# Kernel tuning notes

Hardware: AMD Instinct MI355X
Metric: run time of the kernel (lower is better)

The kernel has to match this reference:

```python
import jax, jax.numpy as jnp
import numpy as np


def setup_inputs() -> dict:
    key = jax.random.key(0)
    k1, k2 = jax.random.split(key)
    B, N, D = 256, 50000, 2048
    queries = jax.random.normal(k1, (B, D), dtype=jnp.float32)
    bank = jax.random.normal(k2, (N, D), dtype=jnp.float32)
    return {"queries": queries, "bank": bank}


def reference(queries, bank):
    # Cosine similarity of every query against every bank row, fused as one
    # GEMM + row-norm scaling (original repeats the query N times per item
    # in a Python loop; math is identical).
    eps = jnp.float32(1e-12)
    q_norm = jnp.sqrt(jnp.sum(queries * queries, axis=1, keepdims=True))  # [B,1]
    b_norm = jnp.sqrt(jnp.sum(bank * bank, axis=1))                       # [N]
    dots = jnp.einsum('bd,nd->bn', queries, bank)                         # [B,N]
    scores = dots / jnp.maximum(q_norm * b_norm[None, :], eps)
    best_idx = jnp.argmax(scores, axis=1)  # retrieval result per batch item
    return best_idx, scores
```

## Files before the change

### kernel.cpp

```cpp
#include <hip/hip_runtime.h>
#include <stdint.h>

#define MQ 256
#define NB 50000
#define KD 2048
#define BN 64
#define BK 64
#define KT (KD / BK)
#define NBLK ((NB + BN - 1) / BN)

typedef __attribute__((ext_vector_type(8))) short bf16x8;
typedef __attribute__((ext_vector_type(4))) float f32x4;

__device__ __forceinline__ unsigned int pack_bf16(float a, float b) {
  unsigned int ua = __float_as_uint(a);
  ua += 0x7fffu + ((ua >> 16) & 1u);
  unsigned int ub = __float_as_uint(b);
  ub += 0x7fffu + ((ub >> 16) & 1u);
  return (ua >> 16) | (ub & 0xffff0000u);
}

__device__ __forceinline__ unsigned int ordf(float f) {
  unsigned int u = __float_as_uint(f);
  return (u & 0x80000000u) ? ~u : (u | 0x80000000u);
}
__device__ __forceinline__ float deordf(unsigned int e) {
  unsigned int u = (e & 0x80000000u) ? (e ^ 0x80000000u) : ~e;
  return __uint_as_float(u);
}

__device__ __forceinline__ float wave_sum(float v) {
#pragma unroll
  for (int o = 32; o > 0; o >>= 1) v += __shfl_down(v, o, 64);
  return v;
}

__global__ __launch_bounds__(256) void prep_q(const float* __restrict__ q,
                                              unsigned short* __restrict__ qbf,
                                              float* __restrict__ qn) {
  const int b = blockIdx.x, tid = threadIdx.x;
  const float* row = q + (size_t)b * KD;
  float4 v0 = *(const float4*)(row + tid * 8);
  float4 v1 = *(const float4*)(row + tid * 8 + 4);
  float sq = v0.x * v0.x + v0.y * v0.y + v0.z * v0.z + v0.w * v0.w +
             v1.x * v1.x + v1.y * v1.y + v1.z * v1.z + v1.w * v1.w;
  uint4 o;
  o.x = pack_bf16(v0.x, v0.y);
  o.y = pack_bf16(v0.z, v0.w);
  o.z = pack_bf16(v1.x, v1.y);
  o.w = pack_bf16(v1.z, v1.w);
  *(uint4*)(qbf + (size_t)b * KD + tid * 8) = o;
  sq = wave_sum(sq);
  __shared__ float s4[4];
  if ((tid & 63) == 0) s4[tid >> 6] = sq;
  __syncthreads();
  if (tid == 0) qn[b] = sqrtf(s4[0] + s4[1] + s4[2] + s4[3]);
}

__global__ __launch_bounds__(256, 3) void gemm_scores(
    const float* __restrict__ bank, const unsigned short* __restrict__ qbf,
    const float* __restrict__ qn, float* __restrict__ out_scores,
    unsigned long long* __restrict__ bm) {
  __shared__ alignas(16) unsigned short As[MQ * BK];
  __shared__ alignas(16) unsigned short Bs[BN * BK];
  __shared__ float qn_s[MQ];
  __shared__ float bsq_s[256];
  __shared__ float bn_s[BN];

  const int tid = threadIdx.x;
  const int w = tid >> 6;
  const int lane = tid & 63;
  const int n0 = blockIdx.x * BN;

  qn_s[tid] = qn[tid];

  f32x4 acc[4][4] = {};

  const int br = tid >> 2;
  const int bseg = (tid & 3) * 16;
  int brow = n0 + br;
  if (brow >= NB) brow = NB - 1;
  const float* bsrc = bank + (size_t)brow * KD + bseg;

  const int a_row_in_grp = lane >> 3;
  const int a_colb = (lane & 7) * 8;
  float bsq = 0.f;

  float4 f0 = *(const float4*)(bsrc);
  float4 f1 = *(const float4*)(bsrc + 4);
  float4 f2 = *(const float4*)(bsrc + 8);
  float4 f3 = *(const float4*)(bsrc + 12);

  for (int kt = 0; kt < KT; ++kt) {
    const int k0 = kt * BK;
#pragma unroll
    for (int i = 0; i < 8; ++i) {
      const int row = w * 64 + i * 8 + a_row_in_grp;
      const unsigned short* src = qbf + (size_t)row * KD + k0 + a_colb;
      unsigned short* dst = &As[row * BK + a_colb];
      __builtin_amdgcn_global_load_lds(
          (const __attribute__((address_space(1))) unsigned int*)src,
          (__attribute__((address_space(3))) unsigned int*)dst, 16, 0, 0);
    }
    bsq += f0.x * f0.x + f0.y * f0.y + f0.z * f0.z + f0.w * f0.w +
           f1.x * f1.x + f1.y * f1.y + f1.z * f1.z + f1.w * f1.w +
           f2.x * f2.x + f2.y * f2.y + f2.z * f2.z + f2.w * f2.w +
           f3.x * f3.x + f3.y * f3.y + f3.z * f3.z + f3.w * f3.w;
    uint4 p0, p1;
    p0.x = pack_bf16(f0.x, f0.y);
    p0.y = pack_bf16(f0.z, f0.w);
    p0.z = pack_bf16(f1.x, f1.y);
    p0.w = pack_bf16(f1.z, f1.w);
    p1.x = pack_bf16(f2.x, f2.y);
    p1.y = pack_bf16(f2.z, f2.w);
    p1.z = pack_bf16(f3.x, f3.y);
    p1.w = pack_bf16(f3.z, f3.w);
    *(uint4*)&Bs[br * BK + bseg] = p0;
    *(uint4*)&Bs[br * BK + bseg + 8] = p1;
    __syncthreads();
    if (kt + 1 < KT) {
      const float* p = bsrc + (kt + 1) * BK;
      f0 = *(const float4*)(p);
      f1 = *(const float4*)(p + 4);
      f2 = *(const float4*)(p + 8);
      f3 = *(const float4*)(p + 12);
    }
#pragma unroll
    for (int s = 0; s < 2; ++s) {
      bf16x8 af[4], bfv[4];
#pragma unroll
      for (int t = 0; t < 4; ++t) {
        af[t] = *(const bf16x8*)&As[(w * 64 + t * 16 + (lane & 15)) * BK +
                                    s * 32 + (lane >> 4) * 8];
        bfv[t] = *(const bf16x8*)&Bs[(t * 16 + (lane & 15)) * BK + s * 32 +
                                     (lane >> 4) * 8];
      }
#pragma unroll
      for (int tm = 0; tm < 4; ++tm)
#pragma unroll
        for (int tn = 0; tn < 4; ++tn)
          acc[tm][tn] = __builtin_amdgcn_mfma_f32_16x16x32_bf16(
              af[tm], bfv[tn], acc[tm][tn], 0, 0, 0);
    }
    __syncthreads();
  }

  bsq_s[tid] = bsq;
  __syncthreads();
  if (tid < BN)
    bn_s[tid] = sqrtf(bsq_s[tid * 4] + bsq_s[tid * 4 + 1] + bsq_s[tid * 4 + 2] +
                      bsq_s[tid * 4 + 3]);
  __syncthreads();

  const int quad = lane >> 4, nl = lane & 15;
#pragma unroll
  for (int tm = 0; tm < 4; ++tm) {
#pragma unroll
    for (int r = 0; r < 4; ++r) {
      const int m = w * 64 + tm * 16 + quad * 4 + r;
      const float qm = qn_s[m];
      unsigned long long best = 0ull;
#pragma unroll
      for (int tn = 0; tn < 4; ++tn) {
        const int gn = n0 + tn * 16 + nl;
        if (gn < NB) {
          const float sc =
              acc[tm][tn][r] / fmaxf(qm * bn_s[tn * 16 + nl], 1e-12f);
          out_scores[(size_t)m * NB + gn] = sc;
          const unsigned long long pk =
              ((unsigned long long)ordf(sc) << 32) | (unsigned int)gn;
          best = pk > best ? pk : best;
        }
      }
#pragma unroll
      for (int mask = 1; mask < 16; mask <<= 1) {
        const unsigned long long o = __shfl_xor(best, mask, 64);
        best = o > best ? o : best;
      }
      if (nl == 0) bm[(size_t)m * NBLK + blockIdx.x] = best;
    }
  }
}

__global__ __launch_bounds__(256) void argmax_rescue(
    const unsigned long long* __restrict__ bm, const float* __restrict__ scores,
    const float* __restrict__ q, const float* __restrict__ bank,
    float* __restrict__ out_idx) {
  const int b = blockIdx.x, tid = threadIdx.x;
  const int w = tid >> 6, lane = tid & 63;
  const unsigned long long* rbm = bm + (size_t)b * NBLK;

  unsigned long long pmax = 0ull;
  for (int i = tid; i < NBLK; i += 256) {
    const unsigned long long v = rbm[i];
    pmax = v > pmax ? v : pmax;
  }
#pragma unroll
  for (int o = 32; o > 0; o >>= 1) {
    const unsigned long long v = __shfl_down(pmax, o, 64);
    pmax = v > pmax ? v : pmax;
  }
  __shared__ unsigned long long red[4];
  if (lane == 0) red[w] = pmax;
  __syncthreads();
  unsigned long long gmax = red[0];
#pragma unroll
  for (int i = 1; i < 4; ++i) gmax = red[i] > gmax ? red[i] : gmax;
  const float thr = deordf((unsigned int)(gmax >> 32)) - 2e-3f;

  __shared__ int cand[64];
  __shared__ int cnt;
  if (tid == 0) cnt = 0;
  __syncthreads();
  const float* srow = scores + (size_t)b * NB;
  for (int i = tid; i < NBLK; i += 256) {
    const float bmf = deordf((unsigned int)(rbm[i] >> 32));
    if (bmf >= thr) {
      const int base = i * BN;
      const int lim = min(BN, NB - base);
      for (int j = 0; j < lim; ++j) {
        if (srow[base + j] >= thr) {
          const int c = atomicAdd(&cnt, 1);
          if (c < 64) cand[c] = base + j;
        }
      }
    }
  }
  __syncthreads();
  const int nc = min(cnt, 64);

  __shared__ float dd[4], ss[4];
  float best = -1e30f;
  int bidx = 0x7fffffff;
  const float* qrow = q + (size_t)b * KD;
  for (int c = 0; c < nc; ++c) {
    const int idx = cand[c];
    const float* brow = bank + (size_t)idx * KD;
    float d = 0.f, s = 0.f;
#pragma unroll
    for (int j = 0; j < 8; ++j) {
      const float bv = brow[tid * 8 + j];
      const float qv = qrow[tid * 8 + j];
      d = fmaf(qv, bv, d);
      s = fmaf(bv, bv, s);
    }
    d = wave_sum(d);
    s = wave_sum(s);
    if (lane == 0) {
      dd[w] = d;
      ss[w] = s;
    }
    __syncthreads();
    const float dt = dd[0] + dd[1] + dd[2] + dd[3];
    const float st = ss[0] + ss[1] + ss[2] + ss[3];
    const float sc = dt / fmaxf(sqrtf(st), 1e-12f);
    if (sc > best || (sc == best && idx < bidx)) {
      best = sc;
      bidx = idx;
    }
    __syncthreads();
  }
  if (tid == 0) out_idx[b] = (float)bidx;
}

extern "C" void kernel_launch(void* const* d_in, const int* in_sizes, int n_in,
                              void* d_out, int out_size, void* d_ws,
                              size_t ws_size, hipStream_t stream) {
  const float* queries = (const float*)d_in[0];
  const float* bank = (const float*)d_in[1];
  float* out = (float*)d_out;
  float* out_scores = out + MQ;

  char* ws = (char*)d_ws;
  unsigned short* qbf = (unsigned short*)ws;
  float* qn = (float*)(ws + (size_t)MQ * KD * 2);
  unsigned long long* bm =
      (unsigned long long*)(ws + (size_t)MQ * KD * 2 + 2048);

  prep_q<<<MQ, 256, 0, stream>>>(queries, qbf, qn);
  gemm_scores<<<NBLK, 256, 0, stream>>>(bank, qbf, qn, out_scores, bm);
  argmax_rescue<<<MQ, 256, 0, stream>>>(bm, out_scores, queries, bank, out);
}
```

Measured before the change: 631.3 us.

## XOR-swizzle A/B LDS tiles and hand-tune waitcnt barriers for prefetch overlap

Applies an XOR swizzle to the LDS layout of the query (A) and bank (B) tiles so the MFMA fragment reads avoid bank conflicts. For A, the global source column is permuted while the LDS destination stays linear. The change also replaces __syncthreads with explicit s_waitcnt plus s_barrier and scheduling fences. This lets the next-iteration bank prefetch loads stay in flight (vmcnt(4)) across the barrier instead of being drained. The handwritten waitcnt counts depend on the compiler's load ordering, which risks a correctness fault if that ordering changes.

Result: no change. 627.9 us (-0.5%).

```diff
diff --git a/kernel.cpp b/kernel.cpp
--- a/kernel.cpp
+++ b/kernel.cpp
@@ -11,6 +11,12 @@
 
 typedef __attribute__((ext_vector_type(8))) short bf16x8;
 typedef __attribute__((ext_vector_type(4))) float f32x4;
+
+#define SFENCE()                       \
+  do {                                 \
+    asm volatile("" ::: "memory");     \
+    __builtin_amdgcn_sched_barrier(0); \
+  } while (0)
 
 __device__ __forceinline__ unsigned int pack_bf16(float a, float b) {
   unsigned int ua = __float_as_uint(a);
@@ -78,12 +84,14 @@
 
   const int br = tid >> 2;
   const int bseg = (tid & 3) * 16;
+  const int bkey = (br & 7) * 8;
+  const int be0 = bseg ^ bkey;
   int brow = n0 + br;
   if (brow >= NB) brow = NB - 1;
   const float* bsrc = bank + (size_t)brow * KD + bseg;
 
-  const int a_row_in_grp = lane >> 3;
-  const int a_colb = (lane & 7) * 8;
+  const int arow = lane >> 3;
+  const int acs = ((lane & 7) ^ arow) * 8;
   float bsq = 0.f;
 
   float4 f0 = *(const float4*)(bsrc);
@@ -93,15 +101,17 @@
 
   for (int kt = 0; kt < KT; ++kt) {
     const int k0 = kt * BK;
+    SFENCE();
 #pragma unroll
     for (int i = 0; i < 8; ++i) {
-      const int row = w * 64 + i * 8 + a_row_in_grp;
-      const unsigned short* src = qbf + (size_t)row * KD + k0 + a_colb;
-      unsigned short* dst = &As[row * BK + a_colb];
+      const int row = w * 64 + i * 8 + arow;
+      const unsigned short* src = qbf + (size_t)row * KD + k0 + acs;
+      unsigned short* dst = &As[row * BK + (lane & 7) * 8];
       __builtin_amdgcn_global_load_lds(
           (const __attribute__((address_space(1))) unsigned int*)src,
           (__attribute__((address_space(3))) unsigned int*)dst, 16, 0, 0);
     }
+    SFENCE();
     bsq += f0.x * f0.x + f0.y * f0.y + f0.z * f0.z + f0.w * f0.w +
            f1.x * f1.x + f1.y * f1.y + f1.z * f1.z + f1.w * f1.w +
            f2.x * f2.x + f2.y * f2.y + f2.z * f2.z + f2.w * f2.w +
@@ -115,25 +125,28 @@
     p1.y = pack_bf16(f2.z, f2.w);
     p1.z = pack_bf16(f3.x, f3.y);
     p1.w = pack_bf16(f3.z, f3.w);
-    *(uint4*)&Bs[br * BK + bseg] = p0;
-    *(uint4*)&Bs[br * BK + bseg + 8] = p1;
-    __syncthreads();
+    *(uint4*)&Bs[br * BK + be0] = p0;
+    *(uint4*)&Bs[br * BK + (be0 ^ 8)] = p1;
     if (kt + 1 < KT) {
       const float* p = bsrc + (kt + 1) * BK;
       f0 = *(const float4*)(p);
       f1 = *(const float4*)(p + 4);
       f2 = *(const float4*)(p + 8);
       f3 = *(const float4*)(p + 12);
-    }
+      asm volatile("s_waitcnt vmcnt(4) lgkmcnt(0)" ::: "memory");
+    } else {
+      asm volatile("s_waitcnt vmcnt(0) lgkmcnt(0)" ::: "memory");
+    }
+    __builtin_amdgcn_s_barrier();
+    SFENCE();
 #pragma unroll
     for (int s = 0; s < 2; ++s) {
+      const int kx = (s * 32 + (lane >> 4) * 8) ^ ((lane & 7) * 8);
       bf16x8 af[4], bfv[4];
 #pragma unroll
       for (int t = 0; t < 4; ++t) {
-        af[t] = *(const bf16x8*)&As[(w * 64 + t * 16 + (lane & 15)) * BK +
-                                    s * 32 + (lane >> 4) * 8];
-        bfv[t] = *(const bf16x8*)&Bs[(t * 16 + (lane & 15)) * BK + s * 32 +
-                                     (lane >> 4) * 8];
+        af[t] = *(const bf16x8*)&As[(w * 64 + t * 16 + (lane & 15)) * BK + kx];
+        bfv[t] = *(const bf16x8*)&Bs[(t * 16 + (lane & 15)) * BK + kx];
       }
 #pragma unroll
       for (int tm = 0; tm < 4; ++tm)
@@ -142,7 +155,9 @@
           acc[tm][tn] = __builtin_amdgcn_mfma_f32_16x16x32_bf16(
               af[tm], bfv[tn], acc[tm][tn], 0, 0, 0);
     }
-    __syncthreads();
+    asm volatile("s_waitcnt lgkmcnt(0)" ::: "memory");
+    __builtin_amdgcn_s_barrier();
+    SFENCE();
   }
 
   bsq_s[tid] = bsq;
```

## Double-buffer bank tiles, swizzle LDS, load query fragments directly from global

Applied to the files above, without the earlier changes.

The GEMM main loop now uses a ping-pong LDS buffer for the bf16 bank tile, with one barrier per k-step instead of two. The bank tile layout is XOR-swizzled to reduce LDS bank conflicts. The query operand is no longer staged in LDS; each wave loads its bf16x8 MFMA fragments straight from global memory, which cuts LDS traffic and size but relies on cache hits for data reused across blocks. The rescoring kernel also switches to vectorized float4 loads.

Measured after the change: 689.6 us. 1.09x slower.

```diff
diff --git a/kernel.cpp b/kernel.cpp
--- a/kernel.cpp
+++ b/kernel.cpp
@@ -61,8 +61,7 @@
     const float* __restrict__ bank, const unsigned short* __restrict__ qbf,
     const float* __restrict__ qn, float* __restrict__ out_scores,
     unsigned long long* __restrict__ bm) {
-  __shared__ alignas(16) unsigned short As[MQ * BK];
-  __shared__ alignas(16) unsigned short Bs[BN * BK];
+  __shared__ alignas(16) unsigned short Bs[2][BN * BK];
   __shared__ float qn_s[MQ];
   __shared__ float bsq_s[256];
   __shared__ float bn_s[BN];
@@ -78,30 +77,25 @@
 
   const int br = tid >> 2;
   const int bseg = (tid & 3) * 16;
+  const int be0 = bseg ^ ((br & 7) * 8);
   int brow = n0 + br;
   if (brow >= NB) brow = NB - 1;
   const float* bsrc = bank + (size_t)brow * KD + bseg;
 
-  const int a_row_in_grp = lane >> 3;
-  const int a_colb = (lane & 7) * 8;
+  const int quad4 = lane >> 4;
+  const unsigned short* abase[4];
+#pragma unroll
+  for (int t = 0; t < 4; ++t)
+    abase[t] = qbf + (size_t)(w * 64 + t * 16 + (lane & 15)) * KD + quad4 * 8;
+
   float bsq = 0.f;
-
-  float4 f0 = *(const float4*)(bsrc);
-  float4 f1 = *(const float4*)(bsrc + 4);
-  float4 f2 = *(const float4*)(bsrc + 8);
-  float4 f3 = *(const float4*)(bsrc + 12);
-
-  for (int kt = 0; kt < KT; ++kt) {
-    const int k0 = kt * BK;
-#pragma unroll
-    for (int i = 0; i < 8; ++i) {
-      const int row = w * 64 + i * 8 + a_row_in_grp;
-      const unsigned short* src = qbf + (size_t)row * KD + k0 + a_colb;
-      unsigned short* dst = &As[row * BK + a_colb];
-      __builtin_amdgcn_global_load_lds(
-          (const __attribute__((address_space(1))) unsigned int*)src,
-          (__attribute__((address_space(3))) unsigned int*)dst, 16, 0, 0);
-    }
+  float4 f0, f1, f2, f3;
+
+  f0 = *(const float4*)(bsrc);
+  f1 = *(const float4*)(bsrc + 4);
+  f2 = *(const float4*)(bsrc + 8);
+  f3 = *(const float4*)(bsrc + 12);
+  {
     bsq += f0.x * f0.x + f0.y * f0.y + f0.z * f0.z + f0.w * f0.w +
            f1.x * f1.x + f1.y * f1.y + f1.z * f1.z + f1.w * f1.w +
            f2.x * f2.x + f2.y * f2.y + f2.z * f2.z + f2.w * f2.w +
@@ -115,25 +109,28 @@
     p1.y = pack_bf16(f2.z, f2.w);
     p1.z = pack_bf16(f3.x, f3.y);
     p1.w = pack_bf16(f3.z, f3.w);
-    *(uint4*)&Bs[br * BK + bseg] = p0;
-    *(uint4*)&Bs[br * BK + bseg + 8] = p1;
-    __syncthreads();
-    if (kt + 1 < KT) {
-      const float* p = bsrc + (kt + 1) * BK;
-      f0 = *(const float4*)(p);
-      f1 = *(const float4*)(p + 4);
-      f2 = *(const float4*)(p + 8);
-      f3 = *(const float4*)(p + 12);
-    }
+    *(uint4*)&Bs[0][br * BK + be0] = p0;
+    *(uint4*)&Bs[0][br * BK + (be0 ^ 8)] = p1;
+  }
+  __syncthreads();
+  {
+    const float* p = bsrc + BK;
+    f0 = *(const float4*)(p);
+    f1 = *(const float4*)(p + 4);
+    f2 = *(const float4*)(p + 8);
+    f3 = *(const float4*)(p + 12);
+  }
+
+  for (int kt = 0; kt < KT; ++kt) {
+    const int p = kt & 1;
 #pragma unroll
     for (int s = 0; s < 2; ++s) {
+      const int kx = (s * 32 + quad4 * 8) ^ ((lane & 7) * 8);
       bf16x8 af[4], bfv[4];
 #pragma unroll
       for (int t = 0; t < 4; ++t) {
-        af[t] = *(const bf16x8*)&As[(w * 64 + t * 16 + (lane & 15)) * BK +
-                                    s * 32 + (lane >> 4) * 8];
-        bfv[t] = *(const bf16x8*)&Bs[(t * 16 + (lane & 15)) * BK + s * 32 +
-                                     (lane >> 4) * 8];
+        af[t] = *(const bf16x8*)(abase[t] + kt * BK + s * 32);
+        bfv[t] = *(const bf16x8*)&Bs[p][(t * 16 + (lane & 15)) * BK + kx];
       }
 #pragma unroll
       for (int tm = 0; tm < 4; ++tm)
@@ -142,9 +139,34 @@
           acc[tm][tn] = __builtin_amdgcn_mfma_f32_16x16x32_bf16(
               af[tm], bfv[tn], acc[tm][tn], 0, 0, 0);
     }
-    __syncthreads();
-  }
-
+    if (kt + 1 < KT) {
+      bsq += f0.x * f0.x + f0.y * f0.y + f0.z * f0.z + f0.w * f0.w +
+             f1.x * f1.x + f1.y * f1.y + f1.z * f1.z + f1.w * f1.w +
+             f2.x * f2.x + f2.y * f2.y + f2.z * f2.z + f2.w * f2.w +
+             f3.x * f3.x + f3.y * f3.y + f3.z * f3.z + f3.w * f3.w;
+      uint4 p0, p1;
+      p0.x = pack_bf16(f0.x, f0.y);
+      p0.y = pack_bf16(f0.z, f0.w);
+      p0.z = pack_bf16(f1.x, f1.y);
+      p0.w = pack_bf16(f1.z, f1.w);
+      p1.x = pack_bf16(f2.x, f2.y);
+      p1.y = pack_bf16(f2.z, f2.w);
+      p1.z = pack_bf16(f3.x, f3.y);
+      p1.w = pack_bf16(f3.z, f3.w);
+      *(uint4*)&Bs[p ^ 1][br * BK + be0] = p0;
+      *(uint4*)&Bs[p ^ 1][br * BK + (be0 ^ 8)] = p1;
+      __syncthreads();
+      if (kt + 2 < KT) {
+        const float* pp = bsrc + (kt + 2) * BK;
+        f0 = *(const float4*)(pp);
+        f1 = *(const float4*)(pp + 4);
+        f2 = *(const float4*)(pp + 8);
+        f3 = *(const float4*)(pp + 12);
+      }
+    }
+  }
+
+  __syncthreads();
   bsq_s[tid] = bsq;
   __syncthreads();
   if (tid < BN)
@@ -236,14 +258,27 @@
   for (int c = 0; c < nc; ++c) {
     const int idx = cand[c];
     const float* brow = bank + (size_t)idx * KD;
+    float4 bv0 = *(const float4*)(brow + tid * 8);
+    float4 bv1 = *(const float4*)(brow + tid * 8 + 4);
+    float4 qv0 = *(const float4*)(qrow + tid * 8);
+    float4 qv1 = *(const float4*)(qrow + tid * 8 + 4);
     float d = 0.f, s = 0.f;
-#pragma unroll
-    for (int j = 0; j < 8; ++j) {
-      const float bv = brow[tid * 8 + j];
-      const float qv = qrow[tid * 8 + j];
-      d = fmaf(qv, bv, d);
-      s = fmaf(bv, bv, s);
-    }
+    d = fmaf(qv0.x, bv0.x, d);
+    s = fmaf(bv0.x, bv0.x, s);
+    d = fmaf(qv0.y, bv0.y, d);
+    s = fmaf(bv0.y, bv0.y, s);
+    d = fmaf(qv0.z, bv0.z, d);
+    s = fmaf(bv0.z, bv0.z, s);
+    d = fmaf(qv0.w, bv0.w, d);
+    s = fmaf(bv0.w, bv0.w, s);
+    d = fmaf(qv1.x, bv1.x, d);
+    s = fmaf(bv1.x, bv1.x, s);
+    d = fmaf(qv1.y, bv1.y, d);
+    s = fmaf(bv1.y, bv1.y, s);
+    d = fmaf(qv1.z, bv1.z, d);
+    s = fmaf(bv1.z, bv1.z, s);
+    d = fmaf(qv1.w, bv1.w, d);
+    s = fmaf(bv1.w, bv1.w, s);
     d = wave_sum(d);
     s = wave_sum(s);
     if (lane == 0) {
```
